# Optimization experiments

Hardware: AMD Instinct MI355X
Metric: run time of the kernel (lower is better)

Reference implementation:

```python
import jax, jax.numpy as jnp
import numpy as np

HIDDEN = 1024
HEADS = 16
HEAD_DIM = HIDDEN // HEADS
LN_EPS = 1e-5


def setup_inputs() -> dict:
    key = jax.random.key(0)
    ks = jax.random.split(key, 8)
    B, S = 4, 2048
    s = 1.0 / np.sqrt(HIDDEN)
    return {
        "x": jax.random.normal(ks[0], (B, S, HIDDEN), dtype=jnp.float32),
        "Wq": jax.random.normal(ks[1], (HIDDEN, HIDDEN), dtype=jnp.float32) * s,
        "bq": jax.random.normal(ks[2], (HIDDEN,), dtype=jnp.float32) * 0.01,
        "Wk": jax.random.normal(ks[3], (HIDDEN, HIDDEN), dtype=jnp.float32) * s,
        "bk": jax.random.normal(ks[4], (HIDDEN,), dtype=jnp.float32) * 0.01,
        "Wv": jax.random.normal(ks[5], (HIDDEN, HIDDEN), dtype=jnp.float32) * s,
        "bv": jax.random.normal(ks[6], (HIDDEN,), dtype=jnp.float32) * 0.01,
        "gamma": jnp.ones((HIDDEN,), dtype=jnp.float32),
        "beta": jnp.zeros((HIDDEN,), dtype=jnp.float32),
    }


def reference(x, Wq, bq, Wk, bk, Wv, bv, gamma, beta):
    B, S, H = x.shape
    # LayerNorm
    mu = jnp.mean(x, axis=-1, keepdims=True)
    var = jnp.mean(jnp.square(x - mu), axis=-1, keepdims=True)
    xn = (x - mu) / jnp.sqrt(var + LN_EPS) * gamma + beta
    # QKV projections -> [B, heads, S, head_dim]
    def split_heads(t):
        return t.reshape(B, S, HEADS, HEAD_DIM).transpose(0, 2, 1, 3)
    q = split_heads(xn @ Wq + bq)
    k = split_heads(xn @ Wk + bk)
    v = split_heads(xn @ Wv + bv)
    scores = jnp.einsum("bhqd,bhkd->bhqk", q, k) / np.sqrt(HEAD_DIM)
    probs = jax.nn.softmax(scores, axis=-1)
    attended = jnp.einsum("bhqk,bhkd->bhqd", probs, v)
    attended = attended.transpose(0, 2, 1, 3).reshape(B, S, H)
    # residual (dropout = 0.0 / eval mode is identity)
    return xn + attended
```

## Files before the change

kernel.cpp:

```cpp
#include <hip/hip_runtime.h>
#include <hip/hip_bf16.h>

#define HIDDEN 1024
#define HEADS 16
#define HEAD_DIM 64
#define SEQ 2048
#define BATCH 4

typedef __attribute__((ext_vector_type(8))) short bf16x8;
typedef __attribute__((ext_vector_type(4))) float f32x4;
typedef __attribute__((ext_vector_type(16))) float f32x16;
typedef __attribute__((ext_vector_type(4))) short short4v;

static __device__ __forceinline__ unsigned short f2bf(float f) {
  union { float f; unsigned u; } u;
  u.f = f;
  unsigned r = u.u + 0x7fffu + ((u.u >> 16) & 1u);
  return (unsigned short)(r >> 16);
}

static __device__ __forceinline__ unsigned packtr(float lo, float hi) {
  union { float f; unsigned u; } a, b;
  a.f = lo; b.f = hi;
#if __has_builtin(__builtin_amdgcn_perm)
  return __builtin_amdgcn_perm(b.u, a.u, 0x07060302u);
#else
  return (b.u & 0xFFFF0000u) | (a.u >> 16);
#endif
}

static __device__ __forceinline__ bf16x8 frag4(unsigned u0, unsigned u1,
                                               unsigned u2, unsigned u3) {
  union { unsigned u[4]; bf16x8 v; } t;
  t.u[0] = u0; t.u[1] = u1; t.u[2] = u2; t.u[3] = u3;
  return t.v;
}

static __device__ __forceinline__ float fexp2(float x) {
#if __has_builtin(__builtin_amdgcn_exp2f)
  return __builtin_amdgcn_exp2f(x);
#else
  return exp2f(x);
#endif
}

typedef const __attribute__((address_space(1))) unsigned int* gp1_t;
typedef __attribute__((address_space(3))) unsigned int* lp3_t;
static __device__ __forceinline__ void gload_lds16(const void* g, void* l) {
  __builtin_amdgcn_global_load_lds((gp1_t)g, (lp3_t)l, 16, 0, 0);
}

__global__ __launch_bounds__(256) void wtrans_kernel(
    const float* __restrict__ Wq, const float* __restrict__ Wk,
    const float* __restrict__ Wv, unsigned short* __restrict__ Wt) {
  __shared__ float tile[64][65];
  int z = blockIdx.z;
  const float* W = (z == 0) ? Wq : (z == 1) ? Wk : Wv;
  int k0 = blockIdx.x * 64, n0 = blockIdx.y * 64;
  int tid = threadIdx.x;
  int tr = tid >> 4;
  int tc = tid & 15;
#pragma unroll
  for (int p = 0; p < 4; ++p) {
    int kk = p * 16 + tr;
    float4 v = *(const float4*)(W + (size_t)(k0 + kk) * HIDDEN + n0 + tc * 4);
    tile[kk][tc * 4 + 0] = v.x; tile[kk][tc * 4 + 1] = v.y;
    tile[kk][tc * 4 + 2] = v.z; tile[kk][tc * 4 + 3] = v.w;
  }
  __syncthreads();
  unsigned short* op = Wt + (size_t)z * HIDDEN * HIDDEN;
#pragma unroll
  for (int p = 0; p < 4; ++p) {
    int nn = p * 16 + tr;
    short4v o;
    o.x = (short)f2bf(tile[tc * 4 + 0][nn]);
    o.y = (short)f2bf(tile[tc * 4 + 1][nn]);
    o.z = (short)f2bf(tile[tc * 4 + 2][nn]);
    o.w = (short)f2bf(tile[tc * 4 + 3][nn]);
    *(short4v*)(op + (size_t)(n0 + nn) * HIDDEN + k0 + tc * 4) = o;
  }
}

__global__ __launch_bounds__(256) void ln_kernel(
    const float* __restrict__ x, const float* __restrict__ gamma,
    const float* __restrict__ beta, float* __restrict__ out,
    unsigned short* __restrict__ xnb) {
  int row = blockIdx.x;
  int tid = threadIdx.x;
  const float4* xr = (const float4*)(x + (size_t)row * HIDDEN);
  float4 v = xr[tid];
  float s = v.x + v.y + v.z + v.w;
  float sq = v.x * v.x + v.y * v.y + v.z * v.z + v.w * v.w;
#pragma unroll
  for (int off = 32; off >= 1; off >>= 1) {
    s += __shfl_xor(s, off);
    sq += __shfl_xor(sq, off);
  }
  __shared__ float red[8];
  int wave = tid >> 6, lane = tid & 63;
  if (lane == 0) { red[wave] = s; red[4 + wave] = sq; }
  __syncthreads();
  s = red[0] + red[1] + red[2] + red[3];
  sq = red[4] + red[5] + red[6] + red[7];
  float mu = s * (1.0f / HIDDEN);
  float var = sq * (1.0f / HIDDEN) - mu * mu;
  float rstd = rsqrtf(var + 1e-5f);
  float4 g = ((const float4*)gamma)[tid];
  float4 bt = ((const float4*)beta)[tid];
  float4 o;
  o.x = (v.x - mu) * rstd * g.x + bt.x;
  o.y = (v.y - mu) * rstd * g.y + bt.y;
  o.z = (v.z - mu) * rstd * g.z + bt.z;
  o.w = (v.w - mu) * rstd * g.w + bt.w;
  ((float4*)(out + (size_t)row * HIDDEN))[tid] = o;
  short4v p;
  p.x = (short)f2bf(o.x); p.y = (short)f2bf(o.y);
  p.z = (short)f2bf(o.z); p.w = (short)f2bf(o.w);
  *((short4v*)(xnb + (size_t)row * HIDDEN) + tid) = p;
}

__global__ __launch_bounds__(256) void qkv_gemm(
    const unsigned short* __restrict__ xnb, const unsigned short* __restrict__ Wt,
    const float* __restrict__ bq, const float* __restrict__ bk,
    const float* __restrict__ bv, unsigned short* __restrict__ qO,
    unsigned short* __restrict__ kO, unsigned short* __restrict__ vtO) {
  __shared__ unsigned short As[2][128 * 64];
  __shared__ unsigned short Bs[2][128 * 64];
  int z = blockIdx.z;
  int m0 = blockIdx.x * 128;
  int n0 = blockIdx.y * 128;
  int tid = threadIdx.x;
  int wave = tid >> 6, lane = tid & 63;
  int lr = lane & 15, g = lane >> 4;
  int wm = wave >> 1, wn = wave & 1;
  const unsigned short* Ab = xnb + (size_t)m0 * HIDDEN;
  const unsigned short* Bb = Wt + (size_t)z * HIDDEN * HIDDEN + (size_t)n0 * HIDDEN;
  int srow = wave * 8 + (lane >> 3);
  int scol = ((lane & 7) ^ (lane >> 3)) << 3;
  f32x4 acc[4][4];
#pragma unroll
  for (int i = 0; i < 4; ++i)
#pragma unroll
    for (int j = 0; j < 4; ++j) acc[i][j] = (f32x4){0.f, 0.f, 0.f, 0.f};

#pragma unroll
  for (int i = 0; i < 4; ++i) {
    int row = i * 32 + srow;
    gload_lds16(Ab + (size_t)row * HIDDEN + scol, &As[0][(i * 32 + wave * 8) * 64]);
    gload_lds16(Bb + (size_t)row * HIDDEN + scol, &Bs[0][(i * 32 + wave * 8) * 64]);
  }
  __syncthreads();

#pragma unroll 1
  for (int t = 0; t < 16; ++t) {
    int cur = t & 1;
    if (t < 15) {
      int k1 = (t + 1) * 64;
#pragma unroll
      for (int i = 0; i < 4; ++i) {
        int row = i * 32 + srow;
        gload_lds16(Ab + (size_t)row * HIDDEN + k1 + scol, &As[cur ^ 1][(i * 32 + wave * 8) * 64]);
        gload_lds16(Bb + (size_t)row * HIDDEN + k1 + scol, &Bs[cur ^ 1][(i * 32 + wave * 8) * 64]);
      }
    }
    bf16x8 aF[4][2], bF[4][2];
#pragma unroll
    for (int mb = 0; mb < 4; ++mb) {
      int row = wm * 64 + mb * 16 + lr;
#pragma unroll
      for (int ks = 0; ks < 2; ++ks)
        aF[mb][ks] = *(const bf16x8*)&As[cur][row * 64 + (((ks * 4 + g) ^ (row & 7)) << 3)];
    }
#pragma unroll
    for (int nb = 0; nb < 4; ++nb) {
      int row = wn * 64 + nb * 16 + lr;
#pragma unroll
      for (int ks = 0; ks < 2; ++ks)
        bF[nb][ks] = *(const bf16x8*)&Bs[cur][row * 64 + (((ks * 4 + g) ^ (row & 7)) << 3)];
    }
#pragma unroll
    for (int ks = 0; ks < 2; ++ks)
#pragma unroll
      for (int mb = 0; mb < 4; ++mb)
#pragma unroll
        for (int nb = 0; nb < 4; ++nb)
          acc[mb][nb] = __builtin_amdgcn_mfma_f32_16x16x32_bf16(aF[mb][ks], bF[nb][ks], acc[mb][nb], 0, 0, 0);
    __syncthreads();
  }
  const float* bias = (z == 0) ? bq : (z == 1) ? bk : bv;
  if (z == 2) {
#pragma unroll
    for (int nb = 0; nb < 4; ++nb) {
      int n = n0 + wn * 64 + nb * 16 + lr;
      float bsv = bias[n];
      int h = n >> 6, d = n & 63;
#pragma unroll
      for (int mb = 0; mb < 4; ++mb) {
        int m = m0 + wm * 64 + mb * 16 + g * 4;
        int bb = m >> 11, sIdx = m & 2047;
        short4v pk;
        pk.x = (short)f2bf(acc[mb][nb][0] + bsv);
        pk.y = (short)f2bf(acc[mb][nb][1] + bsv);
        pk.z = (short)f2bf(acc[mb][nb][2] + bsv);
        pk.w = (short)f2bf(acc[mb][nb][3] + bsv);
        *(short4v*)(vtO + (size_t)((bb * HEADS + h) * HEAD_DIM + d) * SEQ + sIdx) = pk;
      }
    }
  } else {
    unsigned short* outp = (z == 0) ? qO : kO;
    float scale = (z == 0) ? 0.18033688011112042f : 1.0f;
#pragma unroll
    for (int nb = 0; nb < 4; ++nb) {
      int n = n0 + wn * 64 + nb * 16 + lr;
      float bsv = bias[n];
      int h = n >> 6, d = n & 63;
#pragma unroll
      for (int mb = 0; mb < 4; ++mb) {
#pragma unroll
        for (int r = 0; r < 4; ++r) {
          int m = m0 + wm * 64 + mb * 16 + g * 4 + r;
          int bb = m >> 11, sIdx = m & 2047;
          unsigned short bits = f2bf((acc[mb][nb][r] + bsv) * scale);
          outp[(size_t)((bb * HEADS + h) * SEQ + sIdx) * HEAD_DIM + d] = bits;
        }
      }
    }
  }
}

__global__ __launch_bounds__(512, 4) void attn_kernel(
    const unsigned short* __restrict__ qB, const unsigned short* __restrict__ kB,
    const unsigned short* __restrict__ vtB, float* __restrict__ out) {
  __shared__ unsigned short Kt[3][64 * 64];
  __shared__ unsigned short Vt[3][64 * 64];
  int orig = blockIdx.y * gridDim.x + blockIdx.x;
  int swz = (orig & 7) * 64 + (orig >> 3);
  int bx = swz & 7;
  int by = swz >> 3;
  int b = by >> 4, hh = by & 15;
  int tid = threadIdx.x, wave = tid >> 6, lane = tid & 63;
  int lq = lane & 31;
  int hf = lane >> 5;
  int q0 = bx * 256 + wave * 32;
  const unsigned short* qh = qB + (size_t)by * SEQ * HEAD_DIM;
  const unsigned short* kh = kB + (size_t)by * SEQ * HEAD_DIM;
  const unsigned short* vh = vtB + (size_t)by * HEAD_DIM * SEQ;

  bf16x8 qF[4];
#pragma unroll
  for (int s = 0; s < 4; ++s)
    qF[s] = *(const bf16x8*)(qh + (size_t)(q0 + lq) * HEAD_DIM + s * 16 + hf * 8);

  int srow = wave * 8 + (lane >> 3);
  int scoff = ((lane & 7) ^ (lane >> 3)) << 3;
  int xorb = (lq & 7) << 4;
  int koff[4];
#pragma unroll
  for (int s = 0; s < 4; ++s)
    koff[s] = (lq * 128 + ((s * 32 + hf * 16) ^ xorb)) >> 1;

  f32x16 o0, o1, ZERO;
#pragma unroll
  for (int r = 0; r < 16; ++r) { o0[r] = 0.f; o1[r] = 0.f; ZERO[r] = 0.f; }
  float lsum = 0.f;

#pragma unroll
  for (int tt = 0; tt < 2; ++tt) {
    gload_lds16(kh + (size_t)(tt * 64 + srow) * HEAD_DIM + scoff, &Kt[tt][wave * 512]);
    gload_lds16(vh + (size_t)srow * SEQ + tt * 64 + scoff, &Vt[tt][wave * 512]);
  }
  asm volatile("s_waitcnt vmcnt(2)" ::: "memory");
  __builtin_amdgcn_s_barrier();
  asm volatile("" ::: "memory");

#pragma unroll 1
  for (int t = 0; t < 32; ++t) {
    int cur = t % 3;
    if (t < 30) {
      int nb = cur + 2; if (nb >= 3) nb -= 3;
      int kv = (t + 2) * 64;
      gload_lds16(kh + (size_t)(kv + srow) * HEAD_DIM + scoff, &Kt[nb][wave * 512]);
      gload_lds16(vh + (size_t)srow * SEQ + kv + scoff, &Vt[nb][wave * 512]);
    }
    const unsigned short* Kb = Kt[cur];
    const unsigned short* Vb = Vt[cur];
    f32x16 sc0, sc1;
    __builtin_amdgcn_s_setprio(1);
    {
      bf16x8 k0 = *(const bf16x8*)&Kb[koff[0]];
      bf16x8 k1 = *(const bf16x8*)&Kb[koff[0] + 2048];
      sc0 = __builtin_amdgcn_mfma_f32_32x32x16_bf16(k0, qF[0], ZERO, 0, 0, 0);
      sc1 = __builtin_amdgcn_mfma_f32_32x32x16_bf16(k1, qF[0], ZERO, 0, 0, 0);
    }
#pragma unroll
    for (int s = 1; s < 4; ++s) {
      bf16x8 k0 = *(const bf16x8*)&Kb[koff[s]];
      bf16x8 k1 = *(const bf16x8*)&Kb[koff[s] + 2048];
      sc0 = __builtin_amdgcn_mfma_f32_32x32x16_bf16(k0, qF[s], sc0, 0, 0, 0);
      sc1 = __builtin_amdgcn_mfma_f32_32x32x16_bf16(k1, qF[s], sc1, 0, 0, 0);
    }
    __builtin_amdgcn_s_setprio(0);
#pragma unroll
    for (int s = 0; s < 4; ++s) {
      float e[8];
#pragma unroll
      for (int j = 0; j < 8; ++j) {
        float scv = (s < 2) ? sc0[8 * s + j] : sc1[8 * (s - 2) + j];
        e[j] = fexp2(scv);
      }
      lsum += ((e[0] + e[1]) + (e[2] + e[3])) + ((e[4] + e[5]) + (e[6] + e[7]));
      unsigned pa0 = packtr(e[0], e[1]);
      unsigned pb0 = packtr(e[2], e[3]);
      unsigned pa1 = packtr(e[4], e[5]);
      unsigned pb1 = packtr(e[6], e[7]);
#if __has_builtin(__builtin_amdgcn_permlane32_swap)
      auto ra = __builtin_amdgcn_permlane32_swap(pa0, pa1, false, false);
      auto rb = __builtin_amdgcn_permlane32_swap(pb0, pb1, false, false);
      bf16x8 pF = frag4(ra[0], rb[0], ra[1], rb[1]);
#else
      unsigned t0 = __shfl_xor(hf ? pa0 : pa1, 32);
      unsigned t1 = __shfl_xor(hf ? pb0 : pb1, 32);
      bf16x8 pF = frag4(hf ? t0 : pa0, hf ? t1 : pb0,
                        hf ? pa1 : t0, hf ? pb1 : t1);
#endif
      bf16x8 v0 = *(const bf16x8*)&Vb[koff[s]];
      bf16x8 v1 = *(const bf16x8*)&Vb[koff[s] + 2048];
      __builtin_amdgcn_s_setprio(1);
      o0 = __builtin_amdgcn_mfma_f32_32x32x16_bf16(v0, pF, o0, 0, 0, 0);
      o1 = __builtin_amdgcn_mfma_f32_32x32x16_bf16(v1, pF, o1, 0, 0, 0);
      __builtin_amdgcn_s_setprio(0);
    }
    if (t < 30) {
      asm volatile("s_waitcnt vmcnt(2)" ::: "memory");
    } else {
      asm volatile("s_waitcnt vmcnt(0)" ::: "memory");
    }
    __builtin_amdgcn_s_barrier();
    asm volatile("" ::: "memory");
  }
  lsum += __shfl_xor(lsum, 32);
  float inv = 1.0f / lsum;
  float* orow = out + ((size_t)b * SEQ + q0 + lq) * HIDDEN + hh * HEAD_DIM;
#pragma unroll
  for (int r = 0; r < 16; ++r) {
    int d0 = (r & 3) + 8 * (r >> 2) + 4 * hf;
    orow[d0] += o0[r] * inv;
    orow[32 + d0] += o1[r] * inv;
  }
}

extern "C" void kernel_launch(void* const* d_in, const int* in_sizes, int n_in,
                              void* d_out, int out_size, void* d_ws, size_t ws_size,
                              hipStream_t stream) {
  const float* x     = (const float*)d_in[0];
  const float* Wq    = (const float*)d_in[1];
  const float* bq    = (const float*)d_in[2];
  const float* Wk    = (const float*)d_in[3];
  const float* bk    = (const float*)d_in[4];
  const float* Wv    = (const float*)d_in[5];
  const float* bv    = (const float*)d_in[6];
  const float* gamma = (const float*)d_in[7];
  const float* beta  = (const float*)d_in[8];
  float* out = (float*)d_out;
  char* ws = (char*)d_ws;
  const size_t MB = 1024 * 1024;
  unsigned short* xnb = (unsigned short*)(ws);
  unsigned short* Wt  = (unsigned short*)(ws + 16 * MB);
  unsigned short* qb  = (unsigned short*)(ws + 22 * MB);
  unsigned short* kb  = (unsigned short*)(ws + 38 * MB);
  unsigned short* vtb = (unsigned short*)(ws + 54 * MB);

  hipLaunchKernelGGL(wtrans_kernel, dim3(16, 16, 3), dim3(256), 0, stream, Wq, Wk, Wv, Wt);
  hipLaunchKernelGGL(ln_kernel, dim3(BATCH * SEQ), dim3(256), 0, stream, x, gamma, beta, out, xnb);
  hipLaunchKernelGGL(qkv_gemm, dim3(64, 8, 3), dim3(256), 0, stream, xnb, Wt, bq, bk, bv, qb, kb, vtb);
  hipLaunchKernelGGL(attn_kernel, dim3(8, 64), dim3(512), 0, stream, qb, kb, vtb, out);
}
```

Baseline: 165.9 us.

## Load V fragments directly from global memory and double-buffer only K in LDS

Drops the LDS staging of V^T. Each wave now reads its V MFMA operands straight from global memory into registers every tile. K keeps an LDS double buffer instead of the triple buffer, and the hand-tuned vmcnt waits become __syncthreads. This cuts LDS footprint and LDS traffic, but the eight waves of a block each reload the same V data from global/L2. It also shortens the K prefetch distance and leaves global-load latency less hidden.

```diff
diff --git a/kernel.cpp b/kernel.cpp
--- a/kernel.cpp
+++ b/kernel.cpp
@@ -231,8 +231,7 @@
 __global__ __launch_bounds__(512, 4) void attn_kernel(
     const unsigned short* __restrict__ qB, const unsigned short* __restrict__ kB,
     const unsigned short* __restrict__ vtB, float* __restrict__ out) {
-  __shared__ unsigned short Kt[3][64 * 64];
-  __shared__ unsigned short Vt[3][64 * 64];
+  __shared__ unsigned short Kt[2][64 * 64];
   int orig = blockIdx.y * gridDim.x + blockIdx.x;
   int swz = (orig & 7) * 64 + (orig >> 3);
   int bx = swz & 7;
@@ -259,31 +258,30 @@
   for (int s = 0; s < 4; ++s)
     koff[s] = (lq * 128 + ((s * 32 + hf * 16) ^ xorb)) >> 1;
 
+  const unsigned short* vrow0 = vh + (size_t)lq * SEQ + hf * 8;
+  const unsigned short* vrow1 = vh + (size_t)(32 + lq) * SEQ + hf * 8;
+
   f32x16 o0, o1, ZERO;
 #pragma unroll
   for (int r = 0; r < 16; ++r) { o0[r] = 0.f; o1[r] = 0.f; ZERO[r] = 0.f; }
   float lsum = 0.f;
 
-#pragma unroll
-  for (int tt = 0; tt < 2; ++tt) {
-    gload_lds16(kh + (size_t)(tt * 64 + srow) * HEAD_DIM + scoff, &Kt[tt][wave * 512]);
-    gload_lds16(vh + (size_t)srow * SEQ + tt * 64 + scoff, &Vt[tt][wave * 512]);
-  }
-  asm volatile("s_waitcnt vmcnt(2)" ::: "memory");
-  __builtin_amdgcn_s_barrier();
-  asm volatile("" ::: "memory");
+  gload_lds16(kh + (size_t)srow * HEAD_DIM + scoff, &Kt[0][wave * 512]);
+  __syncthreads();
 
 #pragma unroll 1
   for (int t = 0; t < 32; ++t) {
-    int cur = t % 3;
-    if (t < 30) {
-      int nb = cur + 2; if (nb >= 3) nb -= 3;
-      int kv = (t + 2) * 64;
-      gload_lds16(kh + (size_t)(kv + srow) * HEAD_DIM + scoff, &Kt[nb][wave * 512]);
-      gload_lds16(vh + (size_t)srow * SEQ + kv + scoff, &Vt[nb][wave * 512]);
+    int cur = t & 1;
+    int kv0 = t * 64;
+    if (t < 31)
+      gload_lds16(kh + (size_t)(kv0 + 64 + srow) * HEAD_DIM + scoff, &Kt[cur ^ 1][wave * 512]);
+    bf16x8 vA0[4], vA1[4];
+#pragma unroll
+    for (int s = 0; s < 4; ++s) {
+      vA0[s] = *(const bf16x8*)(vrow0 + kv0 + s * 16);
+      vA1[s] = *(const bf16x8*)(vrow1 + kv0 + s * 16);
     }
     const unsigned short* Kb = Kt[cur];
-    const unsigned short* Vb = Vt[cur];
     f32x16 sc0, sc1;
     __builtin_amdgcn_s_setprio(1);
     {
@@ -323,20 +321,12 @@
       bf16x8 pF = frag4(hf ? t0 : pa0, hf ? t1 : pb0,
                         hf ? pa1 : t0, hf ? pb1 : t1);
 #endif
-      bf16x8 v0 = *(const bf16x8*)&Vb[koff[s]];
-      bf16x8 v1 = *(const bf16x8*)&Vb[koff[s] + 2048];
       __builtin_amdgcn_s_setprio(1);
-      o0 = __builtin_amdgcn_mfma_f32_32x32x16_bf16(v0, pF, o0, 0, 0, 0);
-      o1 = __builtin_amdgcn_mfma_f32_32x32x16_bf16(v1, pF, o1, 0, 0, 0);
+      o0 = __builtin_amdgcn_mfma_f32_32x32x16_bf16(vA0[s], pF, o0, 0, 0, 0);
+      o1 = __builtin_amdgcn_mfma_f32_32x32x16_bf16(vA1[s], pF, o1, 0, 0, 0);
       __builtin_amdgcn_s_setprio(0);
     }
-    if (t < 30) {
-      asm volatile("s_waitcnt vmcnt(2)" ::: "memory");
-    } else {
-      asm volatile("s_waitcnt vmcnt(0)" ::: "memory");
-    }
-    __builtin_amdgcn_s_barrier();
-    asm volatile("" ::: "memory");
+    __syncthreads();
   }
   lsum += __shfl_xor(lsum, 32);
   float inv = 1.0f / lsum;
```

Result: slower. 228.8 us (+37.9%).
